# Kernel optimization log

Hardware: AMD Instinct MI355X
Metric: run time of the kernel (lower is better)

## Reference

```python
import jax, jax.numpy as jnp
import numpy as np

DIM = 768
NUM_HEADS = 12
HEAD_DIM = DIM // NUM_HEADS
SCALE = HEAD_DIM ** (-0.5)


def setup_inputs() -> dict:
    key = jax.random.key(0)
    ks = jax.random.split(key, 8)
    B, Nq, Nk, Nv = 2, 2048, 2048, 2048
    init = 0.02
    return {
        "xq": jax.random.normal(ks[0], (B, Nq, DIM), dtype=jnp.float32),
        "xk": jax.random.normal(ks[1], (B, Nk, DIM), dtype=jnp.float32),
        "xv": jax.random.normal(ks[2], (B, Nv, DIM), dtype=jnp.float32),
        # torch nn.Linear weights are [out_features, in_features]; qkv_bias=False
        "Wq": jax.random.normal(ks[3], (DIM, DIM), dtype=jnp.float32) * init,
        "Wk": jax.random.normal(ks[4], (DIM, DIM), dtype=jnp.float32) * init,
        "Wv": jax.random.normal(ks[5], (DIM, DIM), dtype=jnp.float32) * init,
        "Wp": jax.random.normal(ks[6], (DIM, DIM), dtype=jnp.float32) * init,
        "bp": jax.random.normal(ks[7], (DIM,), dtype=jnp.float32) * init,
    }


def reference(xq, xk, xv, Wq, Wk, Wv, Wp, bp):
    B, Nq, C = xq.shape
    H, D = NUM_HEADS, HEAD_DIM
    # linear projections (torch Linear: x @ W.T), split heads -> [B, H, N, D]
    q = (xq @ Wq.T).reshape(B, Nq, H, D).transpose(0, 2, 1, 3)
    k = (xk @ Wk.T).reshape(B, xk.shape[1], H, D).transpose(0, 2, 1, 3)
    v = (xv @ Wv.T).reshape(B, xv.shape[1], H, D).transpose(0, 2, 1, 3)
    # attention scores [B, H, Nq, Nk]
    attn = jnp.einsum("bhqd,bhkd->bhqk", q, k) * SCALE
    attn = jax.nn.softmax(attn, axis=-1)
    # weighted values -> merge heads [B, Nq, C]
    out = jnp.einsum("bhqk,bhkd->bhqd", attn, v)
    out = out.transpose(0, 2, 1, 3).reshape(B, Nq, C)
    return out @ Wp.T + bp
```

## Files before the change

kernel.cpp:

```cpp
#include <hip/hip_runtime.h>
#include <hip/hip_bf16.h>


#define NSEQ 2048
#define CDIM 768
#define NH   12
#define HD   64
#define MTOT 4096
#define XEL  (MTOT*CDIM)
#define WEL  (CDIM*CDIM)
#define X8   (XEL/8)
#define W8   (WEL/8)
#define QSCALE 0.18033688011112042f

typedef __attribute__((ext_vector_type(8))) short bf16x8;
typedef __attribute__((ext_vector_type(4))) float floatx4;
typedef __attribute__((ext_vector_type(16))) float floatx16;
typedef __attribute__((ext_vector_type(4))) unsigned int uintx4;

static __device__ __forceinline__ unsigned short f2bf(float f) {
  union { float f; unsigned int u; } v; v.f = f;
  return (unsigned short)((v.u + 0x8000u) >> 16);
}
static __device__ __forceinline__ unsigned pk2bf(float a, float b) {
  unsigned ua = __float_as_uint(a) + 0x8000u;
  unsigned ub = __float_as_uint(b) + 0x8000u;
  return __builtin_amdgcn_perm(ub, ua, 0x07060302);
}

static __device__ __forceinline__ void lds16(const void* g, void* l) {
  __builtin_amdgcn_global_load_lds(
      (const __attribute__((address_space(1))) unsigned int*)g,
      (__attribute__((address_space(3))) unsigned int*)l, 16, 0, 0);
}

__global__ __launch_bounds__(256) void cast_all(
    const float* __restrict__ xq, const float* __restrict__ xk,
    const float* __restrict__ xv, const float* __restrict__ wq,
    const float* __restrict__ wk, const float* __restrict__ wv,
    const float* __restrict__ wp,
    unsigned short* __restrict__ Xq, unsigned short* __restrict__ Xk,
    unsigned short* __restrict__ Xv, unsigned short* __restrict__ Wq,
    unsigned short* __restrict__ Wk, unsigned short* __restrict__ Wv,
    unsigned short* __restrict__ Wp) {
  int i = blockIdx.x * 256 + threadIdx.x;
  const float* s; unsigned short* d; int off;
  if (i < 3 * X8) {
    int t = i / X8; off = i - t * X8;
    s = (t == 0) ? xq : (t == 1) ? xk : xv;
    d = (t == 0) ? Xq : (t == 1) ? Xk : Xv;
  } else {
    int j = i - 3 * X8; int t = j / W8; off = j - t * W8;
    s = (t == 0) ? wq : (t == 1) ? wk : (t == 2) ? wv : wp;
    d = (t == 0) ? Wq : (t == 1) ? Wk : (t == 2) ? Wv : Wp;
  }
  const float4* sp = (const float4*)s + (size_t)off * 2;
  float4 a = sp[0], b = sp[1];
  uint4 o;
  o.x = pk2bf(a.x, a.y); o.y = pk2bf(a.z, a.w);
  o.z = pk2bf(b.x, b.y); o.w = pk2bf(b.z, b.w);
  *(uint4*)(d + (size_t)off * 8) = o;
}

__global__ __launch_bounds__(256) void gemm_qkv(
    const unsigned short* __restrict__ Xq, const unsigned short* __restrict__ Xk,
    const unsigned short* __restrict__ Xv, const unsigned short* __restrict__ Wq,
    const unsigned short* __restrict__ Wk, const unsigned short* __restrict__ Wv,
    unsigned short* __restrict__ Qo, unsigned short* __restrict__ Ko,
    unsigned short* __restrict__ Vo) {
  int i0 = blockIdx.x;
  int mg = i0 & 7; int t0 = i0 >> 3;
  int z = t0 % 3; int u = t0 / 3;
  int xn = u & 7, ysub = u >> 3;
  int y = mg * 4 + ysub;
  const unsigned short* A; const unsigned short* B; int am0, bn0, RA;
  if (z == 0)      { A = Xq; B = Wq; am0 = y * 128; bn0 = xn * 96; RA = 128; }
  else if (z == 1) { A = Xk; B = Wk; am0 = y * 128; bn0 = xn * 96; RA = 128; }
  else             { A = Wv; B = Xv; am0 = xn * 96; bn0 = y * 128; RA = 96; }
  __shared__ __align__(16) unsigned short S[224 * 64];
  int tid = threadIdx.x, lane = tid & 63, wave = tid >> 6;
  int quad = lane >> 4, l15 = lane & 15, l7 = l15 & 7;

  const unsigned short* gptr[7]; int ldo[7];
#pragma unroll
  for (int i = 0; i < 7; i++) {
    int idx = i * 256 + tid;
    int row = idx >> 3, c = (idx & 7) ^ (row & 7);
    gptr[i] = (row < RA ? A + (size_t)(am0 + row) * CDIM
                        : B + (size_t)(bn0 + row - RA) * CDIM) + c * 8;
    ldo[i] = idx * 8;
  }
  floatx4 acc[12];
#pragma unroll
  for (int i = 0; i < 12; i++) acc[i] = (floatx4){0.f, 0.f, 0.f, 0.f};

  for (int k0 = 0; k0 < CDIM; k0 += 64) {
#pragma unroll
    for (int i = 0; i < 7; i++) lds16(gptr[i] + k0, &S[ldo[i]]);
    __syncthreads();
    if (z < 2) {
      int wm = (wave >> 1) * 64, wn = (wave & 1) * 48;
#pragma unroll
      for (int ks = 0; ks < 2; ks++) {
        int csw = ((ks * 4 + quad) ^ l7) * 8;
        bf16x8 af[4], bfr[3];
#pragma unroll
        for (int i = 0; i < 4; i++)
          af[i] = *(const bf16x8*)&S[(wm + i * 16 + l15) * 64 + csw];
#pragma unroll
        for (int j = 0; j < 3; j++)
          bfr[j] = *(const bf16x8*)&S[(128 + wn + j * 16 + l15) * 64 + csw];
#pragma unroll
        for (int mi = 0; mi < 4; mi++)
#pragma unroll
          for (int ni = 0; ni < 3; ni++)
            acc[mi * 3 + ni] = __builtin_amdgcn_mfma_f32_16x16x32_bf16(
                af[mi], bfr[ni], acc[mi * 3 + ni], 0, 0, 0);
      }
    } else {
      int wm = (wave & 1) * 48, wn = (wave >> 1) * 64;
#pragma unroll
      for (int ks = 0; ks < 2; ks++) {
        int csw = ((ks * 4 + quad) ^ l7) * 8;
        bf16x8 af[3], bfr[4];
#pragma unroll
        for (int i = 0; i < 3; i++)
          af[i] = *(const bf16x8*)&S[(wm + i * 16 + l15) * 64 + csw];
#pragma unroll
        for (int j = 0; j < 4; j++)
          bfr[j] = *(const bf16x8*)&S[(96 + wn + j * 16 + l15) * 64 + csw];
#pragma unroll
        for (int mi = 0; mi < 3; mi++)
#pragma unroll
          for (int ni = 0; ni < 4; ni++)
            acc[mi * 4 + ni] = __builtin_amdgcn_mfma_f32_16x16x32_bf16(
                af[mi], bfr[ni], acc[mi * 4 + ni], 0, 0, 0);
      }
    }
    __syncthreads();
  }
  if (z < 2) {
    int wm = (wave >> 1) * 64, wn = (wave & 1) * 48;
#pragma unroll
    for (int mi = 0; mi < 4; mi++)
#pragma unroll
      for (int ni = 0; ni < 3; ni++)
#pragma unroll
        for (int r = 0; r < 4; r++) {
          int grow = am0 + wm + mi * 16 + quad * 4 + r;
          int gcol = bn0 + wn + ni * 16 + l15;
          float v = acc[mi * 3 + ni][r];
          int b = grow >> 11, nq = grow & 2047, h = gcol >> 6, dd = gcol & 63;
          if (z == 0)
            Qo[((size_t)(b * NH + h) * NSEQ + nq) * HD + dd] = f2bf(v * QSCALE);
          else
            Ko[((size_t)(b * NH + h) * NSEQ + nq) * HD + dd] = f2bf(v);
        }
  } else {
    int wm = (wave & 1) * 48, wn = (wave >> 1) * 64;
#pragma unroll
    for (int mi = 0; mi < 3; mi++)
#pragma unroll
      for (int ni = 0; ni < 4; ni++)
#pragma unroll
        for (int r = 0; r < 4; r++) {
          int o = am0 + wm + mi * 16 + quad * 4 + r;
          int mgl = bn0 + wn + ni * 16 + l15;
          int b = mgl >> 11, nq = mgl & 2047;
          Vo[((size_t)b * CDIM + o) * NSEQ + nq] = f2bf(acc[mi * 4 + ni][r]);
        }
  }
}

__global__ __launch_bounds__(256, 3) void attn_kernel(
    const unsigned short* __restrict__ Q, const unsigned short* __restrict__ K,
    const unsigned short* __restrict__ Vt, unsigned short* __restrict__ ctx) {
  int i0 = blockIdx.x;
  int xcd = i0 & 7; int t0 = i0 >> 3;
  int bh = xcd * 3 + (t0 >> 5);
  int qt = t0 & 31;
  int tid = threadIdx.x, lane = tid & 63, wave = tid >> 6;
  int half = wave >> 1, qsub = wave & 1;
  int l31 = lane & 31, hi = lane >> 5;
  __shared__ __align__(16) unsigned short Ks[2][64 * 64];
  __shared__ __align__(16) unsigned short Vs[2][64 * 64];
  __shared__ float Lbuf[64];

  const unsigned short* Qg = Q + ((size_t)bh * NSEQ + qt * 64 + qsub * 32) * HD;
  const unsigned short* Kg = K + ((size_t)bh * NSEQ + half * 1024) * HD;
  const unsigned short* Vg = Vt + (size_t)bh * HD * NSEQ + half * 1024;

  bf16x8 qf[4];
#pragma unroll
  for (int dc = 0; dc < 4; dc++)
    qf[dc] = *(const bf16x8*)(Qg + l31 * HD + dc * 16 + hi * 8);

  int tid2 = tid & 127;
  int kgo[4], vgo[4], ldst[4];
#pragma unroll
  for (int i = 0; i < 4; i++) {
    int idx = i * 128 + tid2;
    int R = idx >> 3, c = (idx & 7) ^ (R & 7);
    kgo[i] = R * HD + c * 8;
    vgo[i] = R * NSEQ + c * 8;
    ldst[i] = idx * 8;
  }
  unsigned short* Ksh = Ks[half];
  unsigned short* Vsh = Vs[half];

  floatx16 o[2];
#pragma unroll
  for (int dt = 0; dt < 2; dt++) o[dt] = (floatx16)(0.f);
  float l_acc = 0.f;

  for (int t = 0; t < 16; t++) {
    int k0 = t * 64;
#pragma unroll
    for (int i = 0; i < 4; i++) {
      lds16(Kg + (size_t)k0 * HD + kgo[i], &Ksh[ldst[i]]);
      lds16(Vg + k0 + vgo[i], &Vsh[ldst[i]]);
    }
    __syncthreads();

    bf16x8 kf[2][4];
#pragma unroll
    for (int kb = 0; kb < 2; kb++)
#pragma unroll
      for (int dc = 0; dc < 4; dc++) {
        int R = kb * 32 + l31, c = dc * 2 + hi;
        kf[kb][dc] = *(const bf16x8*)&Ksh[R * 64 + ((c ^ (R & 7)) * 8)];
      }
    bf16x8 vf[2][4];
#pragma unroll
    for (int dt = 0; dt < 2; dt++)
#pragma unroll
      for (int j = 0; j < 4; j++) {
        int R = dt * 32 + l31, c = j * 2 + hi;
        vf[dt][j] = *(const bf16x8*)&Vsh[R * 64 + ((c ^ (R & 7)) * 8)];
      }

#pragma unroll
    for (int kb = 0; kb < 2; kb++) {
      floatx16 st = (floatx16)(0.f);
#pragma unroll
      for (int dc = 0; dc < 4; dc++)
        st = __builtin_amdgcn_mfma_f32_32x32x16_bf16(kf[kb][dc], qf[dc], st, 0, 0, 0);
      float p[16];
#pragma unroll
      for (int r = 0; r < 16; r++) p[r] = __builtin_exp2f(st[r]);
      l_acc += ((p[0] + p[1]) + (p[2] + p[3])) + ((p[4] + p[5]) + (p[6] + p[7])) +
               (((p[8] + p[9]) + (p[10] + p[11])) + ((p[12] + p[13]) + (p[14] + p[15])));
      unsigned w[8];
#pragma unroll
      for (int i = 0; i < 8; i++) w[i] = pk2bf(p[2 * i], p[2 * i + 1]);
#pragma unroll
      for (int kvs = 0; kvs < 2; kvs++) {
        unsigned a0 = w[kvs * 4 + 0], b0 = w[kvs * 4 + 2];
        unsigned a1 = w[kvs * 4 + 1], b1 = w[kvs * 4 + 3];
        asm volatile("v_permlane32_swap_b32 %0, %1" : "+v"(a0), "+v"(b0));
        asm volatile("v_permlane32_swap_b32 %0, %1" : "+v"(a1), "+v"(b1));
        uintx4 pw; pw[0] = a0; pw[1] = a1; pw[2] = b0; pw[3] = b1;
        bf16x8 pb = *(bf16x8*)&pw;
#pragma unroll
        for (int dt = 0; dt < 2; dt++)
          o[dt] = __builtin_amdgcn_mfma_f32_32x32x16_bf16(
              vf[dt][kb * 2 + kvs], pb, o[dt], 0, 0, 0);
      }
    }
    __syncthreads();
  }

  unsigned lu = __float_as_uint(l_acc), lv = __float_as_uint(l_acc);
  asm volatile("v_permlane32_swap_b32 %0, %1" : "+v"(lu), "+v"(lv));
  float lfull = __uint_as_float(lu) + __uint_as_float(lv);

  float* Obuf = (float*)&Ks[0][0];
  int q = qsub * 32 + l31;
  if (half == 1) {
#pragma unroll
    for (int dt = 0; dt < 2; dt++)
#pragma unroll
      for (int rq = 0; rq < 4; rq++) {
        int ch = (dt * 8 + rq * 2 + hi) ^ (l31 & 15);
        floatx4 v4 = {o[dt][rq * 4 + 0], o[dt][rq * 4 + 1],
                      o[dt][rq * 4 + 2], o[dt][rq * 4 + 3]};
        *(floatx4*)&Obuf[q * 64 + ch * 4] = v4;
      }
    if (lane < 32) Lbuf[qsub * 32 + lane] = lfull;
  }
  __syncthreads();
  if (half == 0) {
    int b = bh / NH, h = bh - b * NH;
    float inv = 1.f / (lfull + Lbuf[q]);
    int qrow = qt * 64 + q;
#pragma unroll
    for (int dt = 0; dt < 2; dt++)
#pragma unroll
      for (int rq = 0; rq < 4; rq++) {
        int ch = (dt * 8 + rq * 2 + hi) ^ (l31 & 15);
        floatx4 ob = *(floatx4*)&Obuf[q * 64 + ch * 4];
        float v0 = (o[dt][rq * 4 + 0] + ob[0]) * inv;
        float v1 = (o[dt][rq * 4 + 1] + ob[1]) * inv;
        float v2 = (o[dt][rq * 4 + 2] + ob[2]) * inv;
        float v3 = (o[dt][rq * 4 + 3] + ob[3]) * inv;
        size_t gbase = (size_t)(b * NSEQ + qrow) * CDIM + h * HD +
                       dt * 32 + rq * 8 + hi * 4;
        *(uint2*)&ctx[gbase] = make_uint2(pk2bf(v0, v1), pk2bf(v2, v3));
      }
  }
}

__global__ __launch_bounds__(256) void gemm_out(
    const unsigned short* __restrict__ A, const unsigned short* __restrict__ B,
    const float* __restrict__ bias, float* __restrict__ out) {
  int i0 = blockIdx.x;
  int mg = i0 & 7; int t0 = i0 >> 3;
  int n0 = (t0 & 7) * 96;
  int m0 = (mg * 8 + (t0 >> 3)) * 64;
  __shared__ __align__(16) unsigned short S[160 * 128];
  int tid = threadIdx.x, lane = tid & 63, wave = tid >> 6;
  int quad = lane >> 4, l15 = lane & 15, l7 = l15 & 7;
  int wm = (wave >> 1) * 32, wn = (wave & 1) * 48;
  floatx4 acc[6];
#pragma unroll
  for (int i = 0; i < 6; i++) acc[i] = (floatx4){0.f, 0.f, 0.f, 0.f};

  for (int k0 = 0; k0 < CDIM; k0 += 128) {
#pragma unroll
    for (int i = 0; i < 10; i++) {
      int idx = i * 256 + tid;
      int R = idx >> 4, c4 = idx & 15;
      int cs = (c4 & 8) | ((c4 & 7) ^ (R & 7));
      const unsigned short* g = (R < 64)
          ? A + (size_t)(m0 + R) * CDIM : B + (size_t)(n0 + R - 64) * CDIM;
      lds16(g + k0 + cs * 8, &S[idx * 8]);
    }
    __syncthreads();
#pragma unroll
    for (int ks = 0; ks < 4; ks++) {
      int c = ks * 4 + quad;
      int csw = ((c & 8) | ((c & 7) ^ l7)) * 8;
      bf16x8 af[2], bfr[3];
#pragma unroll
      for (int i = 0; i < 2; i++)
        af[i] = *(const bf16x8*)&S[(wm + i * 16 + l15) * 128 + csw];
#pragma unroll
      for (int j = 0; j < 3; j++)
        bfr[j] = *(const bf16x8*)&S[(64 + wn + j * 16 + l15) * 128 + csw];
#pragma unroll
      for (int mi = 0; mi < 2; mi++)
#pragma unroll
        for (int ni = 0; ni < 3; ni++)
          acc[mi * 3 + ni] = __builtin_amdgcn_mfma_f32_16x16x32_bf16(
              af[mi], bfr[ni], acc[mi * 3 + ni], 0, 0, 0);
    }
    __syncthreads();
  }
  float bv[3];
#pragma unroll
  for (int ni = 0; ni < 3; ni++) bv[ni] = bias[n0 + wn + ni * 16 + l15];
#pragma unroll
  for (int mi = 0; mi < 2; mi++)
#pragma unroll
    for (int ni = 0; ni < 3; ni++)
#pragma unroll
      for (int r = 0; r < 4; r++) {
        int grow = m0 + wm + mi * 16 + quad * 4 + r;
        int gcol = n0 + wn + ni * 16 + l15;
        out[(size_t)grow * CDIM + gcol] = acc[mi * 3 + ni][r] + bv[ni];
      }
}

extern "C" void kernel_launch(void* const* d_in, const int* in_sizes, int n_in,
                              void* d_out, int out_size, void* d_ws, size_t ws_size,
                              hipStream_t stream) {
  const float* xq = (const float*)d_in[0];
  const float* xk = (const float*)d_in[1];
  const float* xv = (const float*)d_in[2];
  const float* wq = (const float*)d_in[3];
  const float* wk = (const float*)d_in[4];
  const float* wv = (const float*)d_in[5];
  const float* wp = (const float*)d_in[6];
  const float* bp = (const float*)d_in[7];
  float* out = (float*)d_out;

  char* p = (char*)d_ws;
  unsigned short* Xq = (unsigned short*)p; p += (size_t)XEL * 2;
  unsigned short* Xk = (unsigned short*)p; p += (size_t)XEL * 2;
  unsigned short* Xv = (unsigned short*)p; p += (size_t)XEL * 2;
  unsigned short* Wq = (unsigned short*)p; p += (size_t)WEL * 2;
  unsigned short* Wk = (unsigned short*)p; p += (size_t)WEL * 2;
  unsigned short* Wv = (unsigned short*)p; p += (size_t)WEL * 2;
  unsigned short* Wp = (unsigned short*)p; p += (size_t)WEL * 2;
  unsigned short* Qb = (unsigned short*)p; p += (size_t)XEL * 2;
  unsigned short* Kb = (unsigned short*)p; p += (size_t)XEL * 2;
  unsigned short* Vb = (unsigned short*)p; p += (size_t)XEL * 2;
  unsigned short* Cx = (unsigned short*)p; p += (size_t)XEL * 2;

  cast_all<<<(3 * X8 + 4 * W8) / 256, 256, 0, stream>>>(
      xq, xk, xv, wq, wk, wv, wp, Xq, Xk, Xv, Wq, Wk, Wv, Wp);

  gemm_qkv<<<768, 256, 0, stream>>>(
      Xq, Xk, Xv, Wq, Wk, Wv, Qb, Kb, Vb);

  attn_kernel<<<768, 256, 0, stream>>>(Qb, Kb, Vb, Cx);

  gemm_out<<<512, 256, 0, stream>>>(Cx, Wp, bp, out);
}
```

Measured before the change: 186.1 us.

## Overlap next-tile global-to-LDS loads with MFMA compute in all three kernels

Each kernel now reads the whole current tile from LDS into registers, waits on lgkmcnt, hits a barrier, and then issues the global_load_lds for the next tile into the same single buffer before running the MFMAs. The intent is to hide global-load latency behind matrix compute without a second LDS buffer, which would cost occupancy. In exchange each thread holds more fragment registers, and the explicit waitcnt, barrier and sched_barrier sequencing has to stay correct or the reused buffer will race.

```diff
diff --git a/kernel.cpp b/kernel.cpp
--- a/kernel.cpp
+++ b/kernel.cpp
@@ -33,6 +33,12 @@
       (const __attribute__((address_space(1))) unsigned int*)g,
       (__attribute__((address_space(3))) unsigned int*)l, 16, 0, 0);
 }
+
+#define LGKM0_SB()  do { asm volatile("s_waitcnt lgkmcnt(0)" ::: "memory"); \
+                         __builtin_amdgcn_sched_barrier(0); } while (0)
+#define VMCNT0()    asm volatile("s_waitcnt vmcnt(0)" ::: "memory")
+#define BARRIER()   __builtin_amdgcn_s_barrier()
+#define SB0()       __builtin_amdgcn_sched_barrier(0)
 
 __global__ __launch_bounds__(256) void cast_all(
     const float* __restrict__ xq, const float* __restrict__ xk,
@@ -94,53 +100,43 @@
 #pragma unroll
   for (int i = 0; i < 12; i++) acc[i] = (floatx4){0.f, 0.f, 0.f, 0.f};
 
-  for (int k0 = 0; k0 < CDIM; k0 += 64) {
-#pragma unroll
-    for (int i = 0; i < 7; i++) lds16(gptr[i] + k0, &S[ldo[i]]);
-    __syncthreads();
-    if (z < 2) {
-      int wm = (wave >> 1) * 64, wn = (wave & 1) * 48;
+#pragma unroll
+  for (int i = 0; i < 7; i++) lds16(gptr[i], &S[ldo[i]]);
+  VMCNT0();
+  BARRIER();
+
+  if (z < 2) {
+    int wm = (wave >> 1) * 64, wn = (wave & 1) * 48;
+    for (int k0 = 0; k0 < CDIM; k0 += 64) {
+      bf16x8 af[2][4], bfr[2][3];
 #pragma unroll
       for (int ks = 0; ks < 2; ks++) {
         int csw = ((ks * 4 + quad) ^ l7) * 8;
-        bf16x8 af[4], bfr[3];
 #pragma unroll
         for (int i = 0; i < 4; i++)
-          af[i] = *(const bf16x8*)&S[(wm + i * 16 + l15) * 64 + csw];
+          af[ks][i] = *(const bf16x8*)&S[(wm + i * 16 + l15) * 64 + csw];
 #pragma unroll
         for (int j = 0; j < 3; j++)
-          bfr[j] = *(const bf16x8*)&S[(128 + wn + j * 16 + l15) * 64 + csw];
+          bfr[ks][j] = *(const bf16x8*)&S[(128 + wn + j * 16 + l15) * 64 + csw];
+      }
+      LGKM0_SB();
+      BARRIER();
+      if (k0 + 64 < CDIM) {
+#pragma unroll
+        for (int i = 0; i < 7; i++) lds16(gptr[i] + k0 + 64, &S[ldo[i]]);
+      }
+      SB0();
+#pragma unroll
+      for (int ks = 0; ks < 2; ks++)
 #pragma unroll
         for (int mi = 0; mi < 4; mi++)
 #pragma unroll
           for (int ni = 0; ni < 3; ni++)
             acc[mi * 3 + ni] = __builtin_amdgcn_mfma_f32_16x16x32_bf16(
-                af[mi], bfr[ni], acc[mi * 3 + ni], 0, 0, 0);
-      }
-    } else {
-      int wm = (wave & 1) * 48, wn = (wave >> 1) * 64;
-#pragma unroll
-      for (int ks = 0; ks < 2; ks++) {
-        int csw = ((ks * 4 + quad) ^ l7) * 8;
-        bf16x8 af[3], bfr[4];
-#pragma unroll
-        for (int i = 0; i < 3; i++)
-          af[i] = *(const bf16x8*)&S[(wm + i * 16 + l15) * 64 + csw];
-#pragma unroll
-        for (int j = 0; j < 4; j++)
-          bfr[j] = *(const bf16x8*)&S[(96 + wn + j * 16 + l15) * 64 + csw];
-#pragma unroll
-        for (int mi = 0; mi < 3; mi++)
-#pragma unroll
-          for (int ni = 0; ni < 4; ni++)
-            acc[mi * 4 + ni] = __builtin_amdgcn_mfma_f32_16x16x32_bf16(
-                af[mi], bfr[ni], acc[mi * 4 + ni], 0, 0, 0);
-      }
-    }
-    __syncthreads();
-  }
-  if (z < 2) {
-    int wm = (wave >> 1) * 64, wn = (wave & 1) * 48;
+                af[ks][mi], bfr[ks][ni], acc[mi * 3 + ni], 0, 0, 0);
+      VMCNT0();
+      BARRIER();
+    }
 #pragma unroll
     for (int mi = 0; mi < 4; mi++)
 #pragma unroll
@@ -158,6 +154,36 @@
         }
   } else {
     int wm = (wave & 1) * 48, wn = (wave >> 1) * 64;
+    for (int k0 = 0; k0 < CDIM; k0 += 64) {
+      bf16x8 af[2][3], bfr[2][4];
+#pragma unroll
+      for (int ks = 0; ks < 2; ks++) {
+        int csw = ((ks * 4 + quad) ^ l7) * 8;
+#pragma unroll
+        for (int i = 0; i < 3; i++)
+          af[ks][i] = *(const bf16x8*)&S[(wm + i * 16 + l15) * 64 + csw];
+#pragma unroll
+        for (int j = 0; j < 4; j++)
+          bfr[ks][j] = *(const bf16x8*)&S[(96 + wn + j * 16 + l15) * 64 + csw];
+      }
+      LGKM0_SB();
+      BARRIER();
+      if (k0 + 64 < CDIM) {
+#pragma unroll
+        for (int i = 0; i < 7; i++) lds16(gptr[i] + k0 + 64, &S[ldo[i]]);
+      }
+      SB0();
+#pragma unroll
+      for (int ks = 0; ks < 2; ks++)
+#pragma unroll
+        for (int mi = 0; mi < 3; mi++)
+#pragma unroll
+          for (int ni = 0; ni < 4; ni++)
+            acc[mi * 4 + ni] = __builtin_amdgcn_mfma_f32_16x16x32_bf16(
+                af[ks][mi], bfr[ks][ni], acc[mi * 4 + ni], 0, 0, 0);
+      VMCNT0();
+      BARRIER();
+    }
 #pragma unroll
     for (int mi = 0; mi < 3; mi++)
 #pragma unroll
@@ -213,15 +239,15 @@
   for (int dt = 0; dt < 2; dt++) o[dt] = (floatx16)(0.f);
   float l_acc = 0.f;
 
+#pragma unroll
+  for (int i = 0; i < 4; i++) {
+    lds16(Kg + kgo[i], &Ksh[ldst[i]]);
+    lds16(Vg + vgo[i], &Vsh[ldst[i]]);
+  }
+  VMCNT0();
+  BARRIER();
+
   for (int t = 0; t < 16; t++) {
-    int k0 = t * 64;
-#pragma unroll
-    for (int i = 0; i < 4; i++) {
-      lds16(Kg + (size_t)k0 * HD + kgo[i], &Ksh[ldst[i]]);
-      lds16(Vg + k0 + vgo[i], &Vsh[ldst[i]]);
-    }
-    __syncthreads();
-
     bf16x8 kf[2][4];
 #pragma unroll
     for (int kb = 0; kb < 2; kb++)
@@ -238,7 +264,17 @@
         int R = dt * 32 + l31, c = j * 2 + hi;
         vf[dt][j] = *(const bf16x8*)&Vsh[R * 64 + ((c ^ (R & 7)) * 8)];
       }
-
+    LGKM0_SB();
+    BARRIER();
+    if (t < 15) {
+      int k0n = (t + 1) * 64;
+#pragma unroll
+      for (int i = 0; i < 4; i++) {
+        lds16(Kg + (size_t)k0n * HD + kgo[i], &Ksh[ldst[i]]);
+        lds16(Vg + k0n + vgo[i], &Vsh[ldst[i]]);
+      }
+    }
+    SB0();
 #pragma unroll
     for (int kb = 0; kb < 2; kb++) {
       floatx16 st = (floatx16)(0.f);
@@ -267,7 +303,8 @@
               vf[dt][kb * 2 + kvs], pb, o[dt], 0, 0, 0);
       }
     }
-    __syncthreads();
+    VMCNT0();
+    BARRIER();
   }
 
   unsigned lu = __float_as_uint(l_acc), lv = __float_as_uint(l_acc);
@@ -325,36 +362,51 @@
 #pragma unroll
   for (int i = 0; i < 6; i++) acc[i] = (floatx4){0.f, 0.f, 0.f, 0.f};
 
+  int sro[10]; const unsigned short* sgp[10];
+#pragma unroll
+  for (int i = 0; i < 10; i++) {
+    int idx = i * 256 + tid;
+    int R = idx >> 4, c4 = idx & 15;
+    int cs = (c4 & 8) | ((c4 & 7) ^ (R & 7));
+    sgp[i] = ((R < 64) ? A + (size_t)(m0 + R) * CDIM
+                       : B + (size_t)(n0 + R - 64) * CDIM) + cs * 8;
+    sro[i] = idx * 8;
+  }
+#pragma unroll
+  for (int i = 0; i < 10; i++) lds16(sgp[i], &S[sro[i]]);
+  VMCNT0();
+  BARRIER();
+
   for (int k0 = 0; k0 < CDIM; k0 += 128) {
-#pragma unroll
-    for (int i = 0; i < 10; i++) {
-      int idx = i * 256 + tid;
-      int R = idx >> 4, c4 = idx & 15;
-      int cs = (c4 & 8) | ((c4 & 7) ^ (R & 7));
-      const unsigned short* g = (R < 64)
-          ? A + (size_t)(m0 + R) * CDIM : B + (size_t)(n0 + R - 64) * CDIM;
-      lds16(g + k0 + cs * 8, &S[idx * 8]);
-    }
-    __syncthreads();
+    bf16x8 af[4][2], bfr[4][3];
 #pragma unroll
     for (int ks = 0; ks < 4; ks++) {
       int c = ks * 4 + quad;
       int csw = ((c & 8) | ((c & 7) ^ l7)) * 8;
-      bf16x8 af[2], bfr[3];
 #pragma unroll
       for (int i = 0; i < 2; i++)
-        af[i] = *(const bf16x8*)&S[(wm + i * 16 + l15) * 128 + csw];
+        af[ks][i] = *(const bf16x8*)&S[(wm + i * 16 + l15) * 128 + csw];
 #pragma unroll
       for (int j = 0; j < 3; j++)
-        bfr[j] = *(const bf16x8*)&S[(64 + wn + j * 16 + l15) * 128 + csw];
+        bfr[ks][j] = *(const bf16x8*)&S[(64 + wn + j * 16 + l15) * 128 + csw];
+    }
+    LGKM0_SB();
+    BARRIER();
+    if (k0 + 128 < CDIM) {
+#pragma unroll
+      for (int i = 0; i < 10; i++) lds16(sgp[i] + k0 + 128, &S[sro[i]]);
+    }
+    SB0();
+#pragma unroll
+    for (int ks = 0; ks < 4; ks++)
 #pragma unroll
       for (int mi = 0; mi < 2; mi++)
 #pragma unroll
         for (int ni = 0; ni < 3; ni++)
           acc[mi * 3 + ni] = __builtin_amdgcn_mfma_f32_16x16x32_bf16(
-              af[mi], bfr[ni], acc[mi * 3 + ni], 0, 0, 0);
-    }
-    __syncthreads();
+              af[ks][mi], bfr[ks][ni], acc[mi * 3 + ni], 0, 0, 0);
+    VMCNT0();
+    BARRIER();
   }
   float bv[3];
 #pragma unroll
```

Measured after the change: 173.5 us. -6.8%, faster.
